# Kernel optimization log

Measured on AMD Instinct MI355X. Metric: run time of the kernel, lower is better.

The kernel has to match this reference:

```python
import math
import jax, jax.numpy as jnp
import numpy as np

RCR = 5.2
RCA = 3.5
ETA_R = 16.0
ETA_A = 8.0
ZETA = 32.0
NUM_SPECIES = 4
SHF_R = jnp.linspace(0.9, RCR, 17)[:-1]                      # [16]
SHF_A = jnp.linspace(0.9, RCA, 5)[:-1]                       # [4]
SHF_Z = (jnp.linspace(0.0, math.pi, 9) + math.pi / 16)[:-1]  # [8]


def _triu_index(num_species):
    i1, i2 = np.triu_indices(num_species)
    pair = np.arange(len(i1))
    ret = np.zeros((num_species, num_species), dtype=np.int32)
    ret[i1, i2] = pair
    ret[i2, i1] = pair
    return jnp.asarray(ret)

TRIU = _triu_index(NUM_SPECIES)  # [S,S] -> pair index in [0, S(S+1)/2)


def setup_inputs() -> dict:
    key = jax.random.key(0)
    k1, k2 = jax.random.split(key)
    species = jax.random.randint(k1, (64, 32), 0, NUM_SPECIES, dtype=jnp.int32)
    # spread atoms over a few Angstrom so neighbor lists are non-trivial
    coordinates = jax.random.normal(k2, (64, 32, 3), dtype=jnp.float32) * 2.0
    return {"species": species, "coordinates": coordinates}


def _cutoff_cosine(d, rc):
    # CutoffCosine: 0.5*cos(pi*d/rc)+0.5 inside cutoff, 0 outside
    return jnp.where(d <= rc, 0.5 * jnp.cos(math.pi * d / rc) + 0.5, 0.0)


def _aev(species, coordinates):
    N, A, _ = coordinates.shape
    S = NUM_SPECIES
    # vec[n,i,j] = coords[n,j] - coords[n,i]
    diff = coordinates[:, None, :, :] - coordinates[:, :, None, :]  # [N,A,A,3]
    d2 = jnp.sum(diff * diff, axis=-1)                              # [N,A,A]
    dist = jnp.sqrt(jnp.where(d2 > 0, d2, 1.0))
    eye = jnp.eye(A, dtype=bool)

    # ---- radial AEV: 0.25 * exp(-EtaR*(d-ShfR)^2) * fc(d), binned by species[j]
    rmask = (~eye) & (dist <= RCR)                                  # [N,A,A]
    fc_r = _cutoff_cosine(dist, RCR)
    g = 0.25 * jnp.exp(-ETA_R * (dist[..., None] - SHF_R) ** 2) * fc_r[..., None]
    g = g * rmask[..., None]                                        # [N,A,A,16]
    sp_onehot = jax.nn.one_hot(species, S, dtype=g.dtype)           # [N,A,S]
    radial = jnp.einsum('nijr,njs->nisr', g, sp_onehot).reshape(N, A, S * 16)

    # ---- angular AEV over triplets (i; j<k), both neighbors within Rca
    amask = (~eye) & (dist <= RCA)                                  # [N,A,A]
    fc_a = _cutoff_cosine(dist, RCA) * amask
    dot = jnp.einsum('nijc,nikc->nijk', diff, diff)                 # [N,A,A,A]
    denom = dist[:, :, :, None] * dist[:, :, None, :]
    cos_ang = jnp.clip(0.95 * dot / jnp.where(denom > 0, denom, 1.0), -0.95, 0.95)
    theta = jnp.arccos(cos_ang)                                     # [N,A,A,A]
    dmean = 0.5 * (dist[:, :, :, None] + dist[:, :, None, :])
    f1 = ((1.0 + jnp.cos(theta[..., None] - SHF_Z)) * 0.5) ** ZETA  # [N,A,A,A,8]
    f2 = jnp.exp(-ETA_A * (dmean[..., None] - SHF_A) ** 2)          # [N,A,A,A,4]
    jk = jnp.arange(A)
    tmask = amask[:, :, :, None] & amask[:, :, None, :] & (jk[:, None] < jk[None, :])
    fc_pair = fc_a[:, :, :, None] * fc_a[:, :, None, :] * tmask
    # sublength ordering: ShfA outer, ShfZ inner (EtaA, Zeta are scalars)
    term = 2.0 * f2[..., :, None] * f1[..., None, :]                # [N,A,A,A,4,8]
    term = (term * fc_pair[..., None, None]).reshape(N, A, A, A, 32)
    pair_idx = TRIU[species[:, :, None], species[:, None, :]]       # [N,A,A]
    pair_oh = jax.nn.one_hot(pair_idx, S * (S + 1) // 2, dtype=term.dtype)
    angular = jnp.einsum('nijku,njkp->nipu', term, pair_oh)
    angular = angular.reshape(N, A, (S * (S + 1) // 2) * 32)

    return jnp.concatenate([radial, angular], axis=-1)              # [N,A,384]


def reference(species, coordinates):
    aev = _aev(species, coordinates)
    return species, aev
```

## Files before the change

### kernel.cpp

```cpp
#include <hip/hip_runtime.h>
#include <math.h>

#define NATOMS 32
#define NMOL   64
#define NPAIRS 496
#define MAXP   466
#define RCRf 5.2f
#define RCAf 3.5f

__global__ __launch_bounds__(384) void aev_kernel(const int* __restrict__ species,
                                                  const float* __restrict__ coords,
                                                  float* __restrict__ out) {
    const int bid = blockIdx.x;
    const int n = bid >> 5;
    const int i = bid & 31;
    const int tid = threadIdx.x;

    __shared__ float4 s_atom[NATOMS];
    __shared__ float  s_fca[NATOMS], s_fcr[NATOMS];
    __shared__ int    s_sp[NATOMS];
    __shared__ float4 s_pd[MAXP];
    __shared__ int    s_cnt[10], s_base[10], s_ofs[10];

    if (tid < 10) s_cnt[tid] = 0;
    if (tid < NATOMS) {
        const float* cb = coords + (size_t)n * NATOMS * 3;
        float dx = cb[tid*3+0] - cb[i*3+0];
        float dy = cb[tid*3+1] - cb[i*3+1];
        float dz = cb[tid*3+2] - cb[i*3+2];
        float d2 = dx*dx + dy*dy + dz*dz;
        float d  = sqrtf(d2 > 0.f ? d2 : 1.f);
        bool self = (tid == i);
        s_fcr[tid] = (!self && d <= RCRf) ? (0.5f*__cosf(((float)M_PI/RCRf)*d) + 0.5f) : 0.f;
        s_fca[tid] = (!self && d <= RCAf) ? (0.5f*__cosf(((float)M_PI/RCAf)*d) + 0.5f) : 0.f;
        s_atom[tid] = make_float4(dx, dy, dz, d);
        s_sp[tid]   = species[n*NATOMS + tid];
    }
    __syncthreads();

    float4 pd0, pd1;
    int px0 = -1, px1 = -1;
    #pragma unroll
    for (int rep = 0; rep < 2; ++rep) {
        int p = tid + rep*384;
        if (p < NPAIRS) {
            float t = sqrtf((float)(3969 - 8*p));
            int j = (int)((63.0f - t) * 0.5f);
            if (j*(63-j)/2 > p) --j;
            if ((j+1)*(62-j)/2 <= p) ++j;
            int k = p - j*(63-j)/2 + j + 1;
            float fc2 = 2.f * s_fca[j] * s_fca[k];
            if (fc2 > 0.f) {
                float4 aj = s_atom[j], ak = s_atom[k];
                float dot = aj.x*ak.x + aj.y*ak.y + aj.z*ak.z;
                float c = 0.95f * dot * __builtin_amdgcn_rcpf(aj.w * ak.w);
                c = fminf(0.95f, fmaxf(-0.95f, c));
                float s = sqrtf(1.f - c*c);
                float dmean = 0.5f * (aj.w + ak.w);
                int sj = s_sp[j], sk = s_sp[k];
                int lo = min(sj, sk), hi = max(sj, sk);
                int px = ((lo*(9-lo)) >> 1) + (hi - lo);
                if (rep == 0) { pd0 = make_float4(c, s, dmean, fc2); px0 = px; }
                else          { pd1 = make_float4(c, s, dmean, fc2); px1 = px; }
                atomicAdd(&s_cnt[px], 1);
            }
        }
    }
    __syncthreads();

    if (tid == 0) {
        int run = 0;
        #pragma unroll
        for (int b = 0; b < 10; ++b) { s_base[b] = run; s_ofs[b] = run; run += s_cnt[b]; }
    }
    __syncthreads();

    if (px0 >= 0) s_pd[atomicAdd(&s_ofs[px0], 1)] = pd0;
    if (px1 >= 0) s_pd[atomicAdd(&s_ofs[px1], 1)] = pd1;
    __syncthreads();

    float* oa = out + NMOL*NATOMS + (size_t)bid * 384;

    if (tid < 320) {
        const int b = tid >> 5;
        const int a = (tid >> 3) & 3;
        const int z = tid & 7;
        const float sha  = 0.9f + 0.65f * (float)a;
        const float zang = (float)z * ((float)M_PI/8.f) + (float)M_PI/16.f;
        const float czv = __cosf(zang), szv = __sinf(zang);
        const int p0 = s_base[b];
        const int pe = p0 + s_cnt[b];

        float acc = 0.f;
        int p = p0;
        for (; p + 1 < pe; p += 2) {
            float4 d0 = s_pd[p];
            float4 d1 = s_pd[p+1];
            float dm0 = d0.z - sha;
            float f0  = __expf(-8.f*dm0*dm0) * d0.w;
            float cd0 = d0.x*czv + d0.y*szv;
            float x0  = 0.5f + 0.5f*cd0;
            float q0 = x0*x0; q0 *= q0; q0 *= q0; q0 *= q0; q0 *= q0;
            acc += f0 * q0;
            float dm1 = d1.z - sha;
            float f1  = __expf(-8.f*dm1*dm1) * d1.w;
            float cd1 = d1.x*czv + d1.y*szv;
            float x1  = 0.5f + 0.5f*cd1;
            float q1 = x1*x1; q1 *= q1; q1 *= q1; q1 *= q1; q1 *= q1;
            acc += f1 * q1;
        }
        if (p < pe) {
            float4 d0 = s_pd[p];
            float dm0 = d0.z - sha;
            float f0  = __expf(-8.f*dm0*dm0) * d0.w;
            float cd0 = d0.x*czv + d0.y*szv;
            float x0  = 0.5f + 0.5f*cd0;
            float q0 = x0*x0; q0 *= q0; q0 *= q0; q0 *= q0; q0 *= q0;
            acc += f0 * q0;
        }
        oa[64 + tid] = acc;
    } else {
        const int f  = tid - 320;
        const int rs = f >> 4;
        const float shr = 0.9f + 0.26875f * (float)(f & 15);
        float racc = 0.f;
        #pragma unroll 8
        for (int j = 0; j < NATOMS; ++j) {
            float d = s_atom[j].w, fr = s_fcr[j];
            float dmr = d - shr;
            racc += (s_sp[j] == rs) ? 0.25f * __expf(-16.f*dmr*dmr) * fr : 0.f;
        }
        oa[f] = racc;
        if (f == 0) out[bid] = (float)s_sp[i];
    }
}

extern "C" void kernel_launch(void* const* d_in, const int* in_sizes, int n_in,
                              void* d_out, int out_size, void* d_ws, size_t ws_size,
                              hipStream_t stream) {
    const int*   species = (const int*)d_in[0];
    const float* coords  = (const float*)d_in[1];
    float*       out     = (float*)d_out;
    aev_kernel<<<NMOL * NATOMS, 384, 0, stream>>>(species, coords, out);
}
```

Measured before the change: 17.14 us.

## Replace shared-memory atomic binning with wave ballot prefix sums

```diff
diff --git a/kernel.cpp b/kernel.cpp
--- a/kernel.cpp
+++ b/kernel.cpp
@@ -8,21 +8,23 @@
 #define RCRf 5.2f
 #define RCAf 3.5f
 
-__global__ __launch_bounds__(384) void aev_kernel(const int* __restrict__ species,
+__global__ __launch_bounds__(512) void aev_kernel(const int* __restrict__ species,
                                                   const float* __restrict__ coords,
                                                   float* __restrict__ out) {
     const int bid = blockIdx.x;
     const int n = bid >> 5;
     const int i = bid & 31;
     const int tid = threadIdx.x;
+    const int wv = tid >> 6;
+    const int lane = tid & 63;
 
     __shared__ float4 s_atom[NATOMS];
     __shared__ float  s_fca[NATOMS], s_fcr[NATOMS];
     __shared__ int    s_sp[NATOMS];
     __shared__ float4 s_pd[MAXP];
-    __shared__ int    s_cnt[10], s_base[10], s_ofs[10];
+    __shared__ int    s_wc[8][10];
+    __shared__ int    s_tot[10], s_base[10];
 
-    if (tid < 10) s_cnt[tid] = 0;
     if (tid < NATOMS) {
         const float* cb = coords + (size_t)n * NATOMS * 3;
         float dx = cb[tid*3+0] - cb[i*3+0];
@@ -38,45 +40,58 @@
     }
     __syncthreads();
 
-    float4 pd0, pd1;
-    int px0 = -1, px1 = -1;
-    #pragma unroll
-    for (int rep = 0; rep < 2; ++rep) {
-        int p = tid + rep*384;
-        if (p < NPAIRS) {
-            float t = sqrtf((float)(3969 - 8*p));
-            int j = (int)((63.0f - t) * 0.5f);
-            if (j*(63-j)/2 > p) --j;
-            if ((j+1)*(62-j)/2 <= p) ++j;
-            int k = p - j*(63-j)/2 + j + 1;
-            float fc2 = 2.f * s_fca[j] * s_fca[k];
-            if (fc2 > 0.f) {
-                float4 aj = s_atom[j], ak = s_atom[k];
-                float dot = aj.x*ak.x + aj.y*ak.y + aj.z*ak.z;
-                float c = 0.95f * dot * __builtin_amdgcn_rcpf(aj.w * ak.w);
-                c = fminf(0.95f, fmaxf(-0.95f, c));
-                float s = sqrtf(1.f - c*c);
-                float dmean = 0.5f * (aj.w + ak.w);
-                int sj = s_sp[j], sk = s_sp[k];
-                int lo = min(sj, sk), hi = max(sj, sk);
-                int px = ((lo*(9-lo)) >> 1) + (hi - lo);
-                if (rep == 0) { pd0 = make_float4(c, s, dmean, fc2); px0 = px; }
-                else          { pd1 = make_float4(c, s, dmean, fc2); px1 = px; }
-                atomicAdd(&s_cnt[px], 1);
-            }
+    float4 pd;
+    int px = -1;
+    if (tid < NPAIRS) {
+        float t = sqrtf((float)(3969 - 8*tid));
+        int j = (int)((63.0f - t) * 0.5f);
+        if (j*(63-j)/2 > tid) --j;
+        if ((j+1)*(62-j)/2 <= tid) ++j;
+        int k = tid - j*(63-j)/2 + j + 1;
+        float fc2 = 2.f * s_fca[j] * s_fca[k];
+        if (fc2 > 0.f) {
+            float4 aj = s_atom[j], ak = s_atom[k];
+            float dot = aj.x*ak.x + aj.y*ak.y + aj.z*ak.z;
+            float c = 0.95f * dot * __builtin_amdgcn_rcpf(aj.w * ak.w);
+            c = fminf(0.95f, fmaxf(-0.95f, c));
+            float s = sqrtf(1.f - c*c);
+            float dmean = 0.5f * (aj.w + ak.w);
+            int sj = s_sp[j], sk = s_sp[k];
+            int lo = min(sj, sk), hi = max(sj, sk);
+            px = ((lo*(9-lo)) >> 1) + (hi - lo);
+            pd = make_float4(c, s, dmean, fc2);
         }
     }
-    __syncthreads();
 
-    if (tid == 0) {
-        int run = 0;
-        #pragma unroll
-        for (int b = 0; b < 10; ++b) { s_base[b] = run; s_ofs[b] = run; run += s_cnt[b]; }
+    const unsigned long long ltm = (lane == 63) ? ~0ull >> 1
+                                                : ((1ull << lane) - 1ull);
+    int myprefix = 0;
+    #pragma unroll
+    for (int b = 0; b < 10; ++b) {
+        unsigned long long m = __ballot(px == b);
+        if (px == b)   myprefix = (int)__popcll(m & ltm);
+        if (lane == b) s_wc[wv][b] = (int)__popcll(m);
     }
     __syncthreads();
-
-    if (px0 >= 0) s_pd[atomicAdd(&s_ofs[px0], 1)] = pd0;
-    if (px1 >= 0) s_pd[atomicAdd(&s_ofs[px1], 1)] = pd1;
+    if (tid < 10) {
+        int t = 0;
+        #pragma unroll
+        for (int w = 0; w < 8; ++w) t += s_wc[w][tid];
+        s_tot[tid] = t;
+    }
+    __syncthreads();
+    if (tid < 10) {
+        int b = 0;
+        for (int t = 0; t < tid; ++t) b += s_tot[t];
+        s_base[tid] = b;
+    }
+    __syncthreads();
+    if (px >= 0) {
+        int pos = s_base[px] + myprefix;
+        #pragma unroll
+        for (int w = 0; w < 7; ++w) if (w < wv) pos += s_wc[w][px];
+        s_pd[pos] = pd;
+    }
     __syncthreads();
 
     float* oa = out + NMOL*NATOMS + (size_t)bid * 384;
@@ -89,7 +104,7 @@
         const float zang = (float)z * ((float)M_PI/8.f) + (float)M_PI/16.f;
         const float czv = __cosf(zang), szv = __sinf(zang);
         const int p0 = s_base[b];
-        const int pe = p0 + s_cnt[b];
+        const int pe = p0 + s_tot[b];
 
         float acc = 0.f;
         int p = p0;
@@ -119,7 +134,7 @@
             acc += f0 * q0;
         }
         oa[64 + tid] = acc;
-    } else {
+    } else if (tid < 384) {
         const int f  = tid - 320;
         const int rs = f >> 4;
         const float shr = 0.9f + 0.26875f * (float)(f & 15);
@@ -141,5 +156,5 @@
     const int*   species = (const int*)d_in[0];
     const float* coords  = (const float*)d_in[1];
     float*       out     = (float*)d_out;
-    aev_kernel<<<NMOL * NATOMS, 384, 0, stream>>>(species, coords, out);
+    aev_kernel<<<NMOL * NATOMS, 512, 0, stream>>>(species, coords, out);
 }
```

Result: slower. 20.27 us (+18.3%).

## Compact angular neighbor list and precompute per-triplet factor records

Applied to the files above, without the earlier changes.

```diff
diff --git a/kernel.cpp b/kernel.cpp
--- a/kernel.cpp
+++ b/kernel.cpp
@@ -3,7 +3,6 @@
 
 #define NATOMS 32
 #define NMOL   64
-#define NPAIRS 496
 #define MAXP   466
 #define RCRf 5.2f
 #define RCAf 3.5f
@@ -19,51 +18,55 @@
     __shared__ float4 s_atom[NATOMS];
     __shared__ float  s_fca[NATOMS], s_fcr[NATOMS];
     __shared__ int    s_sp[NATOMS];
-    __shared__ float4 s_pd[MAXP];
+    __shared__ int    s_nbr[NATOMS];
+    __shared__ int    s_nn;
+    __shared__ __align__(16) float s_rec[MAXP*12];
     __shared__ int    s_cnt[10], s_base[10], s_ofs[10];
 
     if (tid < 10) s_cnt[tid] = 0;
-    if (tid < NATOMS) {
-        const float* cb = coords + (size_t)n * NATOMS * 3;
-        float dx = cb[tid*3+0] - cb[i*3+0];
-        float dy = cb[tid*3+1] - cb[i*3+1];
-        float dz = cb[tid*3+2] - cb[i*3+2];
-        float d2 = dx*dx + dy*dy + dz*dz;
-        float d  = sqrtf(d2 > 0.f ? d2 : 1.f);
-        bool self = (tid == i);
-        s_fcr[tid] = (!self && d <= RCRf) ? (0.5f*__cosf(((float)M_PI/RCRf)*d) + 0.5f) : 0.f;
-        s_fca[tid] = (!self && d <= RCAf) ? (0.5f*__cosf(((float)M_PI/RCAf)*d) + 0.5f) : 0.f;
-        s_atom[tid] = make_float4(dx, dy, dz, d);
-        s_sp[tid]   = species[n*NATOMS + tid];
+
+    if (tid < 64) {
+        float fca_v = 0.f;
+        if (tid < NATOMS) {
+            const float* cb = coords + (size_t)n*NATOMS*3;
+            float dx = cb[tid*3+0] - cb[i*3+0];
+            float dy = cb[tid*3+1] - cb[i*3+1];
+            float dz = cb[tid*3+2] - cb[i*3+2];
+            float d2 = dx*dx + dy*dy + dz*dz;
+            float d  = sqrtf(d2 > 0.f ? d2 : 1.f);
+            bool self = (tid == i);
+            s_fcr[tid] = (!self && d <= RCRf) ? (0.5f*__cosf(((float)M_PI/RCRf)*d) + 0.5f) : 0.f;
+            fca_v      = (!self && d <= RCAf) ? (0.5f*__cosf(((float)M_PI/RCAf)*d) + 0.5f) : 0.f;
+            s_fca[tid]  = fca_v;
+            s_atom[tid] = make_float4(dx, dy, dz, d);
+            s_sp[tid]   = species[n*NATOMS + tid];
+        }
+        unsigned long long m = __ballot(fca_v > 0.f);
+        if (fca_v > 0.f) s_nbr[__popcll(m & ((1ull << tid) - 1ull))] = tid;
+        if (tid == 0) s_nn = (int)__popcll(m);
     }
     __syncthreads();
 
-    float4 pd0, pd1;
-    int px0 = -1, px1 = -1;
+    const int nn  = s_nn;
+    const int cnt = (nn*(nn-1)) >> 1;
+    const int M   = 2*nn - 1;
+
+    int pj[2] = {-1, -1}, pk[2], ppx[2];
     #pragma unroll
     for (int rep = 0; rep < 2; ++rep) {
         int p = tid + rep*384;
-        if (p < NPAIRS) {
-            float t = sqrtf((float)(3969 - 8*p));
-            int j = (int)((63.0f - t) * 0.5f);
-            if (j*(63-j)/2 > p) --j;
-            if ((j+1)*(62-j)/2 <= p) ++j;
-            int k = p - j*(63-j)/2 + j + 1;
-            float fc2 = 2.f * s_fca[j] * s_fca[k];
-            if (fc2 > 0.f) {
-                float4 aj = s_atom[j], ak = s_atom[k];
-                float dot = aj.x*ak.x + aj.y*ak.y + aj.z*ak.z;
-                float c = 0.95f * dot * __builtin_amdgcn_rcpf(aj.w * ak.w);
-                c = fminf(0.95f, fmaxf(-0.95f, c));
-                float s = sqrtf(1.f - c*c);
-                float dmean = 0.5f * (aj.w + ak.w);
-                int sj = s_sp[j], sk = s_sp[k];
-                int lo = min(sj, sk), hi = max(sj, sk);
-                int px = ((lo*(9-lo)) >> 1) + (hi - lo);
-                if (rep == 0) { pd0 = make_float4(c, s, dmean, fc2); px0 = px; }
-                else          { pd1 = make_float4(c, s, dmean, fc2); px1 = px; }
-                atomicAdd(&s_cnt[px], 1);
-            }
+        if (p < cnt) {
+            float t = sqrtf((float)(M*M - 8*p));
+            int jj = (int)(((float)M - t) * 0.5f);
+            while (jj*(2*nn-jj-1)/2 > p) --jj;
+            while ((jj+1)*(2*nn-jj-2)/2 <= p) ++jj;
+            int kk = p - jj*(2*nn-jj-1)/2 + jj + 1;
+            int j = s_nbr[jj], k = s_nbr[kk];
+            int sj = s_sp[j], sk = s_sp[k];
+            int lo = min(sj, sk), hi = max(sj, sk);
+            int px = ((lo*(9-lo)) >> 1) + (hi - lo);
+            pj[rep] = j; pk[rep] = k; ppx[rep] = px;
+            atomicAdd(&s_cnt[px], 1);
         }
     }
     __syncthreads();
@@ -75,8 +78,42 @@
     }
     __syncthreads();
 
-    if (px0 >= 0) s_pd[atomicAdd(&s_ofs[px0], 1)] = pd0;
-    if (px1 >= 0) s_pd[atomicAdd(&s_ofs[px1], 1)] = pd1;
+    const float CZ[8] = { 0.98078528f,  0.83146961f,  0.55557023f,  0.19509032f,
+                         -0.19509032f, -0.55557023f, -0.83146961f, -0.98078528f};
+    const float SZ[8] = { 0.19509032f,  0.55557023f,  0.83146961f,  0.98078528f,
+                          0.98078528f,  0.83146961f,  0.55557023f,  0.19509032f};
+    const float SHA[4] = {0.9f, 1.55f, 2.2f, 2.85f};
+
+    #pragma unroll
+    for (int rep = 0; rep < 2; ++rep) {
+        if (pj[rep] >= 0) {
+            int j = pj[rep], k = pk[rep];
+            float4 aj = s_atom[j], ak = s_atom[k];
+            float fc2 = 2.f * s_fca[j] * s_fca[k];
+            float dot = aj.x*ak.x + aj.y*ak.y + aj.z*ak.z;
+            float c = 0.95f * dot * __builtin_amdgcn_rcpf(aj.w * ak.w);
+            c = fminf(0.95f, fmaxf(-0.95f, c));
+            float s = sqrtf(1.f - c*c);
+            float dmean = 0.5f * (aj.w + ak.w);
+            float f1[8], f2f[4];
+            #pragma unroll
+            for (int z = 0; z < 8; ++z) {
+                float x = 0.5f + 0.5f*(c*CZ[z] + s*SZ[z]);
+                float q = x*x; q *= q; q *= q; q *= q; q *= q;
+                f1[z] = q;
+            }
+            #pragma unroll
+            for (int a = 0; a < 4; ++a) {
+                float dm = dmean - SHA[a];
+                f2f[a] = __expf(-8.f*dm*dm) * fc2;
+            }
+            int slot = atomicAdd(&s_ofs[ppx[rep]], 1);
+            float* r = &s_rec[slot*12];
+            *(float4*)(r+0) = make_float4(f1[0], f1[1], f1[2], f1[3]);
+            *(float4*)(r+4) = make_float4(f1[4], f1[5], f1[6], f1[7]);
+            *(float4*)(r+8) = make_float4(f2f[0], f2f[1], f2f[2], f2f[3]);
+        }
+    }
     __syncthreads();
 
     float* oa = out + NMOL*NATOMS + (size_t)bid * 384;
@@ -85,39 +122,12 @@
         const int b = tid >> 5;
         const int a = (tid >> 3) & 3;
         const int z = tid & 7;
-        const float sha  = 0.9f + 0.65f * (float)a;
-        const float zang = (float)z * ((float)M_PI/8.f) + (float)M_PI/16.f;
-        const float czv = __cosf(zang), szv = __sinf(zang);
         const int p0 = s_base[b];
         const int pe = p0 + s_cnt[b];
-
         float acc = 0.f;
-        int p = p0;
-        for (; p + 1 < pe; p += 2) {
-            float4 d0 = s_pd[p];
-            float4 d1 = s_pd[p+1];
-            float dm0 = d0.z - sha;
-            float f0  = __expf(-8.f*dm0*dm0) * d0.w;
-            float cd0 = d0.x*czv + d0.y*szv;
-            float x0  = 0.5f + 0.5f*cd0;
-            float q0 = x0*x0; q0 *= q0; q0 *= q0; q0 *= q0; q0 *= q0;
-            acc += f0 * q0;
-            float dm1 = d1.z - sha;
-            float f1  = __expf(-8.f*dm1*dm1) * d1.w;
-            float cd1 = d1.x*czv + d1.y*szv;
-            float x1  = 0.5f + 0.5f*cd1;
-            float q1 = x1*x1; q1 *= q1; q1 *= q1; q1 *= q1; q1 *= q1;
-            acc += f1 * q1;
-        }
-        if (p < pe) {
-            float4 d0 = s_pd[p];
-            float dm0 = d0.z - sha;
-            float f0  = __expf(-8.f*dm0*dm0) * d0.w;
-            float cd0 = d0.x*czv + d0.y*szv;
-            float x0  = 0.5f + 0.5f*cd0;
-            float q0 = x0*x0; q0 *= q0; q0 *= q0; q0 *= q0; q0 *= q0;
-            acc += f0 * q0;
-        }
+        #pragma unroll 4
+        for (int p = p0; p < pe; ++p)
+            acc += s_rec[p*12 + z] * s_rec[p*12 + 8 + a];
         oa[64 + tid] = acc;
     } else {
         const int f  = tid - 320;
```

Result: faster. 16.10 us (-6.1%).
